# Performance work log

Measured on AMD Instinct MI355X. Metric: run time of the kernel, lower is better.

The kernel has to match this reference:

```python
import jax, jax.numpy as jnp
import numpy as np

NUM_ITER = 5  # num_iterations
M, N, B = 972, 1944, 8  # check_matrix_row, check_matrix_column, unit_batch_size
ROW_DEG = 8  # check-node degree of the sparse parity matrix


def setup_inputs() -> dict:
    key = jax.random.key(0)
    # sparse binary parity-check matrix H (constant Tanner graph)
    rng = np.random.default_rng(0)
    H = np.zeros((M, N), np.float32)
    for i in range(M):
        H[i, rng.choice(N, ROW_DEG, replace=False)] = 1.0
    soft_input = 2.0 * jax.random.normal(key, (B, N), dtype=jnp.float32)  # channel LLRs
    check_weight = jnp.array([-1.07], dtype=jnp.float32)  # NMS init constant
    return {"soft_input": soft_input, "H": jnp.asarray(H), "check_weight": check_weight}


def _bp_iteration(cv, soft_input, H, check_weight):
    # ---- compute_vc (NMS: bit weight == 1.0) ----
    total = jnp.sum(cv, axis=1) + soft_input              # [B, N]
    vc = total[:, None, :] * H - cv                       # [B, M, N]
    # ---- compute_cv (min-sum branch) ----
    back = jnp.where(H == 0, -1e30 - 1.0, 0.0)[None]      # mask non-edges
    a = jnp.clip(jnp.abs(vc), 0.0, 1e30)
    dec = -a + back
    top2, _ = jax.lax.top_k(dec, 2)                       # [B, M, 2]
    min1 = (-top2[..., 0])[:, :, None] * H                # row min broadcast on edges
    min2 = (-top2[..., 1])[:, :, None] * H                # row second-min
    result = jnp.where(a > min1, min1, min2)              # exclude-self min
    sign_info = (1.0 - H)[None] + vc
    s = jnp.sign(sign_info)
    tot_sign = jnp.prod(s, axis=2)[:, :, None] * H
    result_sign = tot_sign * s                            # exclude-self sign product
    w = jax.nn.softplus(check_weight)                     # scalar NMS factor
    cv_new = result * jax.lax.stop_gradient(result_sign) * w
    return cv_new


def reference(soft_input, H, check_weight):
    Bn, n = soft_input.shape
    m = H.shape[0]
    cv0 = jnp.zeros((Bn, m, n), dtype=soft_input.dtype)

    def body(cv, _):
        return _bp_iteration(cv, soft_input, H, check_weight), None

    cv, _ = jax.lax.scan(body, cv0, None, length=NUM_ITER)
    # marginalize
    soft_output = jnp.sum(cv, axis=1) + soft_input
    return soft_output
```

## Files before the change

### kernel.cpp

```cpp
#include <hip/hip_runtime.h>
#include <math.h>

#define MM 972
#define NN 1944
#define BB 8
#define RD 8
#define NITER 5
#define MAXD 16
#define POISON 0xAAAAAAAAu

__device__ __forceinline__ void emit_edge(int m, int n, int* cnt,
                                          unsigned* __restrict__ col_cnt,
                                          int* __restrict__ row_edges) {
    int j = atomicAdd(cnt, 1);
    unsigned k = atomicAdd(&col_cnt[n], 1u) - POISON;
    if (k > MAXD - 1u) k = MAXD - 1u;
    int kk = (int)k;
    int phys = (((((kk >> 2) + n + (n >> 1)) & 3) << 2) | (kk & 3));
    row_edges[m * RD + j] = n * MAXD + phys;
}

__global__ __launch_bounds__(256) void build_adj(const float* __restrict__ H,
                                                 unsigned* __restrict__ col_cnt,
                                                 int* __restrict__ row_edges) {
    const int m = blockIdx.x;
    __shared__ int cnt;
    if (threadIdx.x == 0) cnt = 0;
    __syncthreads();
    const float4* H4 = (const float4*)(H + (size_t)m * NN);
    for (int q = threadIdx.x; q < NN / 4; q += blockDim.x) {
        float4 h = H4[q];
        int n = 4 * q;
        if (h.x != 0.0f) emit_edge(m, n + 0, &cnt, col_cnt, row_edges);
        if (h.y != 0.0f) emit_edge(m, n + 1, &cnt, col_cnt, row_edges);
        if (h.z != 0.0f) emit_edge(m, n + 2, &cnt, col_cnt, row_edges);
        if (h.w != 0.0f) emit_edge(m, n + 3, &cnt, col_cnt, row_edges);
    }
}

__global__ __launch_bounds__(1024, 1) void decode(const float* __restrict__ soft,
                                                  const float* __restrict__ cwp,
                                                  const unsigned* __restrict__ col_cnt,
                                                  const int* __restrict__ row_edges,
                                                  float* __restrict__ out) {
    __shared__ __align__(16) float cvc[NN * MAXD];
    __shared__ float tot[NN];

    const int b = blockIdx.x;
    const int t = threadIdx.x;
    const float* soft_b = soft + b * NN;

    int rc[RD], rs[RD];
    float cv[RD];
    if (t < MM) {
        const int* rep = row_edges + t * RD;
#pragma unroll
        for (int j = 0; j < RD; ++j) {
            int s = rep[j];
            rs[j] = s;
            rc[j] = s >> 4;
            cv[j] = 0.0f;
        }
    }

    const int n0 = t;
    const int n1 = t + 1024;
    const bool has1 = (n1 < NN);
    const int n1c = has1 ? n1 : 0;
    const float s0 = soft_b[n0];
    const float s1 = has1 ? soft_b[n1] : 0.0f;
    const int g0 = (n0 + (n0 >> 1)) & 3;
    const int g1 = (n1c + (n1c >> 1)) & 3;
    const unsigned d0 = col_cnt[n0] - POISON;
    const unsigned d1 = has1 ? (col_cnt[n1] - POISON) : 0u;
    const int C0 = ((int)min(d0, (unsigned)MAXD) + 3) >> 2;
    const int C1 = ((int)min(d1, (unsigned)MAXD) + 3) >> 2;

    const float w = log1pf(expf(cwp[0]));

    float4* cv4 = (float4*)cvc;
#pragma unroll
    for (int i = 0; i < 8; ++i) {
        int idx = t + i * 1024;
        if (idx < NN * MAXD / 4) cv4[idx] = make_float4(0.f, 0.f, 0.f, 0.f);
    }
    tot[n0] = s0;
    if (has1) tot[n1] = s1;
    __syncthreads();

    for (int it = 0; it < NITER; ++it) {
        if (t < MM) {
            unsigned ab[RD];
            unsigned sg[RD];
            unsigned m1 = 0x7f800000u, m2 = 0x7f800000u, sx = 0u;
#pragma unroll
            for (int j = 0; j < RD; ++j) {
                float vv = tot[rc[j]] - cv[j];
                unsigned u = __float_as_uint(vv);
                sg[j] = u;
                sx ^= u;
                unsigned a = u & 0x7fffffffu;
                ab[j] = a;
                if (a < m1) { m2 = m1; m1 = a; }
                else if (a < m2) { m2 = a; }
            }
            const float we = (m1 == 0u) ? 0.0f : w;
            const unsigned sxb = sx & 0x80000000u;
#pragma unroll
            for (int j = 0; j < RD; ++j) {
                unsigned mag = (ab[j] > m1) ? m1 : m2;
                unsigned sb  = (sg[j] ^ sxb) & 0x80000000u;
                float nc = __uint_as_float(mag | sb) * we;
                cv[j] = nc;
                cvc[rs[j]] = nc;
            }
        }
        __syncthreads();

        float a0 = 0.0f, a1 = 0.0f;
#pragma unroll
        for (int i = 0; i < 4; ++i) {
            if (i < C0) {
                float4 q = cv4[n0 * 4 + ((i + g0) & 3)];
                a0 += (q.x + q.y) + (q.z + q.w);
            }
            if (i < C1) {
                float4 q = cv4[n1c * 4 + ((i + g1) & 3)];
                a1 += (q.x + q.y) + (q.z + q.w);
            }
        }
        const float t0 = s0 + a0;
        const float t1 = s1 + a1;
        if (it == NITER - 1) {
            out[b * NN + n0] = t0;
            if (has1) out[b * NN + n1] = t1;
        } else {
            tot[n0] = t0;
            if (has1) tot[n1] = t1;
            __syncthreads();
        }
    }
}

extern "C" void kernel_launch(void* const* d_in, const int* in_sizes, int n_in,
                              void* d_out, int out_size, void* d_ws, size_t ws_size,
                              hipStream_t stream) {
    const float* soft = (const float*)d_in[0];
    const float* H    = (const float*)d_in[1];
    const float* cw   = (const float*)d_in[2];
    float* out = (float*)d_out;

    unsigned* col_cnt = (unsigned*)d_ws;
    int* row_edges    = (int*)(col_cnt + NN);

    build_adj<<<MM, 256, 0, stream>>>(H, col_cnt, row_edges);
    decode<<<BB, 1024, 0, stream>>>(soft, cw, col_cnt, row_edges, out);
}
```

Measured before the change: 74.86 us.

## Replace per-column edge slot buffer with shared-memory atomic column accumulation

Check-to-variable messages are now summed per column with shared-memory float atomicAdd instead of being written to a padded per-column slot array (NN*16 floats) and reduced in a second pass. This drops the global column-degree counters, the poisoned-counter slot assignment in build_adj, and the large LDS zero-fill. It also shrinks LDS use considerably. In exchange it adds LDS atomic contention and makes the summation order nondeterministic, and the accumulator must be re-zeroed each iteration.

```diff
diff --git a/kernel.cpp b/kernel.cpp
--- a/kernel.cpp
+++ b/kernel.cpp
@@ -6,59 +6,43 @@
 #define BB 8
 #define RD 8
 #define NITER 5
-#define MAXD 16
-#define POISON 0xAAAAAAAAu
-
-__device__ __forceinline__ void emit_edge(int m, int n, int* cnt,
-                                          unsigned* __restrict__ col_cnt,
-                                          int* __restrict__ row_edges) {
-    int j = atomicAdd(cnt, 1);
-    unsigned k = atomicAdd(&col_cnt[n], 1u) - POISON;
-    if (k > MAXD - 1u) k = MAXD - 1u;
-    int kk = (int)k;
-    int phys = (((((kk >> 2) + n + (n >> 1)) & 3) << 2) | (kk & 3));
-    row_edges[m * RD + j] = n * MAXD + phys;
-}
 
 __global__ __launch_bounds__(256) void build_adj(const float* __restrict__ H,
-                                                 unsigned* __restrict__ col_cnt,
                                                  int* __restrict__ row_edges) {
     const int m = blockIdx.x;
     __shared__ int cnt;
     if (threadIdx.x == 0) cnt = 0;
     __syncthreads();
     const float4* H4 = (const float4*)(H + (size_t)m * NN);
+    int* rep = row_edges + m * RD;
     for (int q = threadIdx.x; q < NN / 4; q += blockDim.x) {
         float4 h = H4[q];
         int n = 4 * q;
-        if (h.x != 0.0f) emit_edge(m, n + 0, &cnt, col_cnt, row_edges);
-        if (h.y != 0.0f) emit_edge(m, n + 1, &cnt, col_cnt, row_edges);
-        if (h.z != 0.0f) emit_edge(m, n + 2, &cnt, col_cnt, row_edges);
-        if (h.w != 0.0f) emit_edge(m, n + 3, &cnt, col_cnt, row_edges);
+        if (h.x != 0.0f) rep[atomicAdd(&cnt, 1)] = n + 0;
+        if (h.y != 0.0f) rep[atomicAdd(&cnt, 1)] = n + 1;
+        if (h.z != 0.0f) rep[atomicAdd(&cnt, 1)] = n + 2;
+        if (h.w != 0.0f) rep[atomicAdd(&cnt, 1)] = n + 3;
     }
 }
 
 __global__ __launch_bounds__(1024, 1) void decode(const float* __restrict__ soft,
                                                   const float* __restrict__ cwp,
-                                                  const unsigned* __restrict__ col_cnt,
                                                   const int* __restrict__ row_edges,
                                                   float* __restrict__ out) {
-    __shared__ __align__(16) float cvc[NN * MAXD];
     __shared__ float tot[NN];
+    __shared__ float acc[NN];
 
     const int b = blockIdx.x;
     const int t = threadIdx.x;
     const float* soft_b = soft + b * NN;
 
-    int rc[RD], rs[RD];
+    int rc[RD];
     float cv[RD];
     if (t < MM) {
         const int* rep = row_edges + t * RD;
 #pragma unroll
         for (int j = 0; j < RD; ++j) {
-            int s = rep[j];
-            rs[j] = s;
-            rc[j] = s >> 4;
+            rc[j] = rep[j];
             cv[j] = 0.0f;
         }
     }
@@ -66,26 +50,17 @@
     const int n0 = t;
     const int n1 = t + 1024;
     const bool has1 = (n1 < NN);
-    const int n1c = has1 ? n1 : 0;
     const float s0 = soft_b[n0];
     const float s1 = has1 ? soft_b[n1] : 0.0f;
-    const int g0 = (n0 + (n0 >> 1)) & 3;
-    const int g1 = (n1c + (n1c >> 1)) & 3;
-    const unsigned d0 = col_cnt[n0] - POISON;
-    const unsigned d1 = has1 ? (col_cnt[n1] - POISON) : 0u;
-    const int C0 = ((int)min(d0, (unsigned)MAXD) + 3) >> 2;
-    const int C1 = ((int)min(d1, (unsigned)MAXD) + 3) >> 2;
 
     const float w = log1pf(expf(cwp[0]));
 
-    float4* cv4 = (float4*)cvc;
-#pragma unroll
-    for (int i = 0; i < 8; ++i) {
-        int idx = t + i * 1024;
-        if (idx < NN * MAXD / 4) cv4[idx] = make_float4(0.f, 0.f, 0.f, 0.f);
+    tot[n0] = s0;
+    acc[n0] = 0.0f;
+    if (has1) {
+        tot[n1] = s1;
+        acc[n1] = 0.0f;
     }
-    tot[n0] = s0;
-    if (has1) tot[n1] = s1;
     __syncthreads();
 
     for (int it = 0; it < NITER; ++it) {
@@ -112,31 +87,23 @@
                 unsigned sb  = (sg[j] ^ sxb) & 0x80000000u;
                 float nc = __uint_as_float(mag | sb) * we;
                 cv[j] = nc;
-                cvc[rs[j]] = nc;
+                atomicAdd(&acc[rc[j]], nc);
             }
         }
         __syncthreads();
 
-        float a0 = 0.0f, a1 = 0.0f;
-#pragma unroll
-        for (int i = 0; i < 4; ++i) {
-            if (i < C0) {
-                float4 q = cv4[n0 * 4 + ((i + g0) & 3)];
-                a0 += (q.x + q.y) + (q.z + q.w);
-            }
-            if (i < C1) {
-                float4 q = cv4[n1c * 4 + ((i + g1) & 3)];
-                a1 += (q.x + q.y) + (q.z + q.w);
-            }
-        }
-        const float t0 = s0 + a0;
-        const float t1 = s1 + a1;
+        const float t0 = s0 + acc[n0];
+        const float t1 = has1 ? (s1 + acc[n1]) : 0.0f;
         if (it == NITER - 1) {
             out[b * NN + n0] = t0;
             if (has1) out[b * NN + n1] = t1;
         } else {
             tot[n0] = t0;
-            if (has1) tot[n1] = t1;
+            acc[n0] = 0.0f;
+            if (has1) {
+                tot[n1] = t1;
+                acc[n1] = 0.0f;
+            }
             __syncthreads();
         }
     }
@@ -150,9 +117,8 @@
     const float* cw   = (const float*)d_in[2];
     float* out = (float*)d_out;
 
-    unsigned* col_cnt = (unsigned*)d_ws;
-    int* row_edges    = (int*)(col_cnt + NN);
+    int* row_edges = (int*)d_ws;
 
-    build_adj<<<MM, 256, 0, stream>>>(H, col_cnt, row_edges);
-    decode<<<BB, 1024, 0, stream>>>(soft, cw, col_cnt, row_edges, out);
+    build_adj<<<MM, 256, 0, stream>>>(H, row_edges);
+    decode<<<BB, 1024, 0, stream>>>(soft, cw, row_edges, out);
 }
```

Measured after the change: 117.0 us. +56.3%, slower.
